# Performance work log

Measured on AMD Instinct MI355X. Metric: run time of the kernel, lower is better.

## Reference

```python
import jax, jax.numpy as jnp
import numpy as np

WINDOW_SIZE = 11
SIGMA = 1.5
CHANNEL = 1


def _gaussian_window(window_size, sigma, channel):
    x = np.arange(window_size, dtype=np.float32)
    g = np.exp(-((x - window_size // 2) ** 2) / (2.0 * sigma ** 2))
    g = g / g.sum()
    w2d = np.outer(g, g).astype(np.float32)  # (K, K)
    # torch layout: (channel, 1, K, K) for grouped (depthwise) conv
    return jnp.asarray(np.broadcast_to(w2d, (channel, 1, window_size, window_size)).copy())


def _depthwise_conv(x, window, channel):
    # x: (B, C, H, W), window: (C, 1, K, K); SAME padding, groups=C
    pad = window.shape[-1] // 2
    return jax.lax.conv_general_dilated(
        x, window,
        window_strides=(1, 1),
        padding=[(pad, pad), (pad, pad)],
        dimension_numbers=("NCHW", "OIHW", "NCHW"),
        feature_group_count=channel,
    )


def setup_inputs() -> dict:
    key = jax.random.key(0)
    k1, k2 = jax.random.split(key)
    B, C, H, W = 64, CHANNEL, 512, 512
    img1 = jax.random.uniform(k1, (B, C, H, W), dtype=jnp.float32)
    img2 = jax.random.uniform(k2, (B, C, H, W), dtype=jnp.float32)
    window = _gaussian_window(WINDOW_SIZE, SIGMA, CHANNEL)
    return {"img1": img1, "img2": img2, "window": window}


def reference(img1, img2, window):
    channel = img1.shape[1]
    C1 = 0.01 ** 2
    C2 = 0.03 ** 2
    conv = lambda t: _depthwise_conv(t, window, channel)
    mu1 = conv(img1)
    mu2 = conv(img2)
    mu1_sq = mu1 * mu1
    mu2_sq = mu2 * mu2
    mu1_mu2 = mu1 * mu2
    sigma1_sq = conv(img1 * img1) - mu1_sq
    sigma2_sq = conv(img2 * img2) - mu2_sq
    sigma12 = conv(img1 * img2) - mu1_mu2
    ssim_map = ((2.0 * mu1_mu2 + C1) * (2.0 * sigma12 + C2)) / (
        (mu1_sq + mu2_sq + C1) * (sigma1_sq + sigma2_sq + C2)
    )
    return jnp.mean(ssim_map)  # size_average=True
```

## Files before the change

### kernel.cpp

```cpp
#include <hip/hip_runtime.h>

#define IMG 512
#define BATCH 64
#define RPS 32
#define NSTEP 42
#define WPW 144

typedef float v2f __attribute__((ext_vector_type(2)));

__global__ __launch_bounds__(256, 2) void ssim_dp2_kernel(
    const float* __restrict__ img1, const float* __restrict__ img2,
    const float* __restrict__ window, float* __restrict__ partials)
{
    __shared__ float S[4][2][2][WPW];
    __shared__ float wred[4];

    const int tid   = threadIdx.x;
    const int lane  = tid & 63;
    const int wv    = tid >> 6;
    const int strip = blockIdx.x;
    const int b     = blockIdx.y;
    const int r_base = strip * RPS;
    const int cbase = wv * 128;
    const int c0    = cbase + lane * 2;

    float gw[11];
    #pragma unroll
    for (int k = 0; k < 11; ++k) {
        float s = 0.f;
        #pragma unroll
        for (int j = 0; j < 11; ++j) s += window[k*11 + j];
        gw[k] = __int_as_float(__builtin_amdgcn_readfirstlane(__float_as_int(s)));
    }

    const float* P1 = img1 + (size_t)b * (IMG*IMG);
    const float* P2 = img2 + (size_t)b * (IMG*IMG);

    const bool lh = (lane < 3);
    const bool rh = (lane >= 61);
    const int  lcol = cbase - 6 + 2*lane;
    const int  rcol = cbase + 128 + 2*(lane - 61);
    const bool lok = lh && (lcol >= 0);
    const bool rok = rh && (rcol <= IMG-2);

    auto fetch = [&](int rr, v2f& o1, v2f& o2, v2f& h1_, v2f& h2_) {
        o1=(v2f){0,0}; o2=(v2f){0,0}; h1_=(v2f){0,0}; h2_=(v2f){0,0};
        if (rr >= 0 && rr < IMG) {
            const float* q1 = P1 + (size_t)rr*IMG;
            const float* q2 = P2 + (size_t)rr*IMG;
            o1 = *(const v2f*)(q1 + c0);
            o2 = *(const v2f*)(q2 + c0);
            if (lok) { h1_ = *(const v2f*)(q1 + lcol); h2_ = *(const v2f*)(q2 + lcol); }
            if (rok) { h1_ = *(const v2f*)(q1 + rcol); h2_ = *(const v2f*)(q2 + rcol); }
        }
    };
    auto store = [&](int buf, v2f o1, v2f o2, v2f h1_, v2f h2_) {
        *(v2f*)&S[wv][buf][0][6 + 2*lane] = o1;
        *(v2f*)&S[wv][buf][1][6 + 2*lane] = o2;
        if (lh) { *(v2f*)&S[wv][buf][0][2*lane] = h1_;
                  *(v2f*)&S[wv][buf][1][2*lane] = h2_; }
        if (rh) { *(v2f*)&S[wv][buf][0][134 + 2*(lane-61)] = h1_;
                  *(v2f*)&S[wv][buf][1][134 + 2*(lane-61)] = h2_; }
    };

    v2f pAo1, pAo2, pAh1, pAh2;
    v2f pBo1, pBo2, pBh1, pBh2;

    { v2f o1,o2,e1,e2; fetch(r_base - 5, o1,o2,e1,e2); store(0, o1,o2,e1,e2); }
    fetch(r_base - 4, pAo1,pAo2,pAh1,pAh2);
    fetch(r_base - 3, pBo1,pBo2,pBh1,pBh2);

    v2f acc[11][4];
    #pragma unroll
    for (int s = 0; s < 11; ++s)
        #pragma unroll
        for (int ch = 0; ch < 4; ++ch) acc[s][ch] = (v2f){0.f, 0.f};

    v2f rsum = (v2f){0.f, 0.f};
    const float C1 = 1e-4f, C2 = 9e-4f;

    #pragma unroll 1
    for (int jj = 0; jj < 4; ++jj) {
      #pragma unroll
      for (int u = 0; u < 11; ++u) {
        if (jj < 3 || u < 9) {
          const int t = jj*11 + u;
          const int rr = r_base - 5 + t;

          if ((u & 1) == 0) store((t+1) & 1, pAo1,pAo2,pAh1,pAh2);
          else              store((t+1) & 1, pBo1,pBo2,pBh1,pBh2);

          const float* R1 = &S[wv][t & 1][0][0];
          const float* R2 = &S[wv][t & 1][1][0];
          v2f L1[7], L2[7];
          #pragma unroll
          for (int q = 0; q < 7; ++q) {
            L1[q] = *(const v2f*)&R1[2*lane + 2*q];
            L2[q] = *(const v2f*)&R2[2*lane + 2*q];
          }

          if ((u & 1) == 0) fetch(rr + 3, pAo1,pAo2,pAh1,pAh2);
          else              fetch(rr + 3, pBo1,pBo2,pBh1,pBh2);

          v2f h0 = (v2f){0,0}, hy = (v2f){0,0};
          v2f hs = (v2f){0,0}, hx = (v2f){0,0};
          #pragma unroll
          for (int k = 0; k < 11; ++k) {
            v2f pa, pb;
            if (k & 1) {
              pa = L1[(k+1) >> 1]; pb = L2[(k+1) >> 1];
            } else {
              pa = __builtin_shufflevector(L1[k>>1], L1[(k>>1)+1], 1, 2);
              pb = __builtin_shufflevector(L2[k>>1], L2[(k>>1)+1], 1, 2);
            }
            float w = gw[k];
            h0 += w * pa;
            hy += w * pb;
            hs += w * (pa*pa + pb*pb);
            hx += w * (pa * pb);
          }

          #pragma unroll
          for (int s = 0; s < 11; ++s) {
            const int k = 10 - (((s - u) % 11 + 11) % 11);
            const float w = gw[k];
            acc[s][0] += w * h0;
            acc[s][1] += w * hy;
            acc[s][2] += w * hs;
            acc[s][3] += w * hx;
          }

          if (t >= 10) {
            v2f mu1 = acc[u][0], mu2 = acc[u][1];
            v2f mu1s = mu1*mu1, mu2s = mu2*mu2, mu12 = mu1*mu2;
            v2f sigs  = acc[u][2] - mu1s - mu2s;
            v2f sig12 = acc[u][3] - mu12;
            v2f num = (2.f*mu12 + C1) * (2.f*sig12 + C2);
            v2f den = (mu1s + mu2s + C1) * (sigs + C2);
            rsum.x += num.x * __builtin_amdgcn_rcpf(den.x);
            rsum.y += num.y * __builtin_amdgcn_rcpf(den.y);
          }
          #pragma unroll
          for (int ch = 0; ch < 4; ++ch) acc[u][ch] = (v2f){0.f, 0.f};
        }
      }
      { v2f x;
        x=pAo1; pAo1=pBo1; pBo1=x;  x=pAo2; pAo2=pBo2; pBo2=x;
        x=pAh1; pAh1=pBh1; pBh1=x;  x=pAh2; pAh2=pBh2; pBh2=x; }
    }

    float thr_sum = rsum.x + rsum.y;

    for (int d = 32; d > 0; d >>= 1) thr_sum += __shfl_down(thr_sum, d, 64);
    if (lane == 0) wred[wv] = thr_sum;
    __syncthreads();
    if (tid == 0) {
        float s = wred[0] + wred[1] + wred[2] + wred[3];
        partials[blockIdx.y * 16 + blockIdx.x] = s;
    }
}

__global__ __launch_bounds__(256) void ssim_reduce_kernel(
    const float* __restrict__ partials, int n, float* __restrict__ out)
{
    __shared__ double wsumd[4];
    double s = 0.0;
    for (int i = threadIdx.x; i < n; i += 256) s += (double)partials[i];
    for (int d = 32; d > 0; d >>= 1) s += __shfl_down(s, d, 64);
    int wid = threadIdx.x >> 6, lane = threadIdx.x & 63;
    if (lane == 0) wsumd[wid] = s;
    __syncthreads();
    if (threadIdx.x == 0) {
        double t = wsumd[0] + wsumd[1] + wsumd[2] + wsumd[3];
        out[0] = (float)(t / ((double)BATCH * IMG * IMG));
    }
}

extern "C" void kernel_launch(void* const* d_in, const int* in_sizes, int n_in,
                              void* d_out, int out_size, void* d_ws, size_t ws_size,
                              hipStream_t stream) {
    const float* img1   = (const float*)d_in[0];
    const float* img2   = (const float*)d_in[1];
    const float* window = (const float*)d_in[2];
    float* out = (float*)d_out;
    float* partials = (float*)d_ws;

    dim3 grid(IMG / RPS, BATCH);
    ssim_dp2_kernel<<<grid, dim3(256), 0, stream>>>(img1, img2, window, partials);

    int npart = (IMG / RPS) * BATCH;
    ssim_reduce_kernel<<<1, 256, 0, stream>>>(partials, npart, out);
}
```

Before: 71.47 us.

## Split each block into single-wave blocks to remove cross-wave sync

Each 256-thread block covering four 128-column slices is replaced by a 64-thread block per slice, with the grid gaining a column-block dimension. The per-block shared-memory reduction and __syncthreads are removed, and each wave writes its own partial sum, so the final reduction has four times as many partials. This is meant to give finer-grained scheduling and drop block-level coupling. The cost is more blocks, more launch bookkeeping and a larger final reduction, and occupancy now depends on the launch_bounds(64,4) hint.

```diff
diff --git a/kernel.cpp b/kernel.cpp
--- a/kernel.cpp
+++ b/kernel.cpp
@@ -8,20 +8,18 @@
 
 typedef float v2f __attribute__((ext_vector_type(2)));
 
-__global__ __launch_bounds__(256, 2) void ssim_dp2_kernel(
+__global__ __launch_bounds__(64, 4) void ssim_w1_kernel(
     const float* __restrict__ img1, const float* __restrict__ img2,
     const float* __restrict__ window, float* __restrict__ partials)
 {
-    __shared__ float S[4][2][2][WPW];
-    __shared__ float wred[4];
+    __shared__ float S[2][2][WPW];
 
-    const int tid   = threadIdx.x;
-    const int lane  = tid & 63;
-    const int wv    = tid >> 6;
-    const int strip = blockIdx.x;
-    const int b     = blockIdx.y;
+    const int lane  = threadIdx.x;
+    const int cblk  = blockIdx.x;
+    const int strip = blockIdx.y;
+    const int b     = blockIdx.z;
     const int r_base = strip * RPS;
-    const int cbase = wv * 128;
+    const int cbase = cblk * 128;
     const int c0    = cbase + lane * 2;
 
     float gw[11];
@@ -55,12 +53,12 @@
         }
     };
     auto store = [&](int buf, v2f o1, v2f o2, v2f h1_, v2f h2_) {
-        *(v2f*)&S[wv][buf][0][6 + 2*lane] = o1;
-        *(v2f*)&S[wv][buf][1][6 + 2*lane] = o2;
-        if (lh) { *(v2f*)&S[wv][buf][0][2*lane] = h1_;
-                  *(v2f*)&S[wv][buf][1][2*lane] = h2_; }
-        if (rh) { *(v2f*)&S[wv][buf][0][134 + 2*(lane-61)] = h1_;
-                  *(v2f*)&S[wv][buf][1][134 + 2*(lane-61)] = h2_; }
+        *(v2f*)&S[buf][0][6 + 2*lane] = o1;
+        *(v2f*)&S[buf][1][6 + 2*lane] = o2;
+        if (lh) { *(v2f*)&S[buf][0][2*lane] = h1_;
+                  *(v2f*)&S[buf][1][2*lane] = h2_; }
+        if (rh) { *(v2f*)&S[buf][0][134 + 2*(lane-61)] = h1_;
+                  *(v2f*)&S[buf][1][134 + 2*(lane-61)] = h2_; }
     };
 
     v2f pAo1, pAo2, pAh1, pAh2;
@@ -90,8 +88,8 @@
           if ((u & 1) == 0) store((t+1) & 1, pAo1,pAo2,pAh1,pAh2);
           else              store((t+1) & 1, pBo1,pBo2,pBh1,pBh2);
 
-          const float* R1 = &S[wv][t & 1][0][0];
-          const float* R2 = &S[wv][t & 1][1][0];
+          const float* R1 = &S[t & 1][0][0];
+          const float* R2 = &S[t & 1][1][0];
           v2f L1[7], L2[7];
           #pragma unroll
           for (int q = 0; q < 7; ++q) {
@@ -152,11 +150,9 @@
     float thr_sum = rsum.x + rsum.y;
 
     for (int d = 32; d > 0; d >>= 1) thr_sum += __shfl_down(thr_sum, d, 64);
-    if (lane == 0) wred[wv] = thr_sum;
-    __syncthreads();
-    if (tid == 0) {
-        float s = wred[0] + wred[1] + wred[2] + wred[3];
-        partials[blockIdx.y * 16 + blockIdx.x] = s;
+    if (lane == 0) {
+        int bid = (b * 16 + strip) * 4 + cblk;
+        partials[bid] = thr_sum;
     }
 }
 
@@ -185,9 +181,9 @@
     float* out = (float*)d_out;
     float* partials = (float*)d_ws;
 
-    dim3 grid(IMG / RPS, BATCH);
-    ssim_dp2_kernel<<<grid, dim3(256), 0, stream>>>(img1, img2, window, partials);
+    dim3 grid(4, 16, BATCH);
+    ssim_w1_kernel<<<grid, dim3(64), 0, stream>>>(img1, img2, window, partials);
 
-    int npart = (IMG / RPS) * BATCH;
+    int npart = 4 * 16 * BATCH;
     ssim_reduce_kernel<<<1, 256, 0, stream>>>(partials, npart, out);
 }
```

Result: slower. 131.3 us (+83.8%).
